# Kernel optimization log

Hardware: AMD Instinct MI355X
Metric: run time of the kernel (lower is better)

## Reference

```python
import jax, jax.numpy as jnp
import numpy as np
from jax import lax

KERNEL_SIZE = 15  # conv padding = kernel_size, kernel width = 2*kernel_size+1


def setup_inputs() -> dict:
    key = jax.random.key(0)
    ks = jax.random.split(key, 11)
    B, T, H, U, KN = 32, 2048, 1024, 1024, 32
    inp = {
        "query": jax.random.normal(ks[0], (1, B, H), dtype=jnp.float32),
        "values": jax.random.normal(ks[1], (B, T, H), dtype=jnp.float32),
        "prev_att": jax.random.uniform(ks[2], (B, 1, T), dtype=jnp.float32),
        "W1_w": jax.random.normal(ks[3], (U, H), dtype=jnp.float32) * 0.02,
        "W1_b": jax.random.normal(ks[4], (U,), dtype=jnp.float32) * 0.02,
        "W2_w": jax.random.normal(ks[5], (U, H), dtype=jnp.float32) * 0.02,
        "W2_b": jax.random.normal(ks[6], (U,), dtype=jnp.float32) * 0.02,
        "V_w": jax.random.normal(ks[7], (1, U), dtype=jnp.float32) * 0.02,
        "V_b": jax.random.normal(ks[8], (1,), dtype=jnp.float32) * 0.02,
        "conv_w": jax.random.normal(ks[9], (KN, 1, 2 * KERNEL_SIZE + 1), dtype=jnp.float32) * 0.02,
        "loc_proj_w": jax.random.normal(ks[10], (U, KN), dtype=jnp.float32) * 0.02,
    }
    return inp


def reference(query, values, prev_att, W1_w, W1_b, W2_w, W2_b, V_w, V_b, conv_w, loc_proj_w):
    # query: [1,B,H] -> [B,H]
    q = jnp.squeeze(query, axis=0)
    hidden_with_time_axis = q[:, None, :]  # [B,1,H]

    # location features: Conv1d over prev attention [B,1,T] -> [B,KN,T]
    loc = lax.conv_general_dilated(
        prev_att, conv_w,
        window_strides=(1,),
        padding=[(KERNEL_SIZE, KERNEL_SIZE)],
        dimension_numbers=("NCH", "OIH", "NCH"),
    )
    # project KN -> units: [B,T,U]
    loc_context = jnp.einsum("bkt,uk->btu", loc, loc_proj_w)

    # W1(values) [B,T,U] + W2(query) [B,1,U] + loc_context [B,T,U]
    sum_1 = (jnp.einsum("bth,uh->btu", values, W1_w) + W1_b
             + jnp.einsum("bh,uh->bu", q, W2_w)[:, None, :] + W2_b
             + loc_context)

    # score: [B,T,1]
    score = jnp.einsum("btu,ou->bto", jnp.tanh(sum_1), V_w) + V_b
    attention_weights = jax.nn.softmax(score, axis=1)  # softmax over time
    context_vector = jnp.sum(attention_weights * values, axis=1)  # [B,H]
    return (context_vector, attention_weights, score)
```

## Files before the change

### kernel.cpp

```cpp
#include <hip/hip_runtime.h>
#include <cstdint>
#include <cstddef>

typedef unsigned short ushort_t;
typedef __attribute__((ext_vector_type(8))) short short8;
typedef __attribute__((ext_vector_type(4))) float floatx4;

#define B_   32
#define T_   2048
#define H_   1024
#define U_   1024
#define KN_  32
#define KEXT 1056
#define BT_  (B_ * T_)

__device__ __forceinline__ unsigned short f2bf(float f) {
    union { float f; unsigned int u; } v; v.f = f;
    unsigned int u = v.u;
    return (unsigned short)((u + 0x7FFFu + ((u >> 16) & 1u)) >> 16);
}
__device__ __forceinline__ float bf2f(unsigned short h) {
    union { unsigned int u; float f; } v; v.u = ((unsigned int)h) << 16;
    return v.f;
}
__device__ __forceinline__ float bflo(unsigned int u) {
    union { unsigned int u; float f; } v; v.u = u << 16; return v.f;
}
__device__ __forceinline__ float bfhi(unsigned int u) {
    union { unsigned int u; float f; } v; v.u = u & 0xffff0000u; return v.f;
}
__device__ __forceinline__ void async_cp16(const void* g, void* l) {
    __builtin_amdgcn_global_load_lds(
        (const __attribute__((address_space(1))) unsigned int*)g,
        (__attribute__((address_space(3))) unsigned int*)l, 16, 0, 0);
}
__device__ __forceinline__ float fast_tanh(float x) {
    float e = __expf(2.0f * x);
    return 1.0f - 2.0f * __builtin_amdgcn_rcpf(e + 1.0f);
}

__global__ void pack_values(const float* __restrict__ values, ushort_t* __restrict__ A) {
    const int tid = threadIdx.x;
    const size_t base = (size_t)blockIdx.x * 8;
#pragma unroll
    for (int r = 0; r < 8; ++r) {
        const size_t row = base + r;
        float4 v = reinterpret_cast<const float4*>(values + row * H_)[tid];
        ushort4 o;
        o.x = f2bf(v.x); o.y = f2bf(v.y); o.z = f2bf(v.z); o.w = f2bf(v.w);
        *reinterpret_cast<ushort4*>(A + row * KEXT + tid * 4) = o;
    }
}

__global__ void conv_pack(const float* __restrict__ prev, const float* __restrict__ convw,
                          ushort_t* __restrict__ A) {
    __shared__ float satt[158];
    __shared__ float sw[KN_ * 31];
    const int tid = threadIdx.x;
    const int b = blockIdx.y, t0 = blockIdx.x * 128;
    for (int i = tid; i < 158; i += 256) {
        int t = t0 - 15 + i;
        satt[i] = (t >= 0 && t < T_) ? prev[b * T_ + t] : 0.0f;
    }
    for (int i = tid; i < KN_ * 31; i += 256) sw[i] = convw[i];
    __syncthreads();
    for (int idx = tid; idx < 128 * KN_; idx += 256) {
        const int k = idx & 31, tl = idx >> 5;
        float acc = 0.0f;
#pragma unroll
        for (int j = 0; j < 31; ++j) acc += satt[tl + j] * sw[k * 31 + j];
        A[(size_t)(b * T_ + t0 + tl) * KEXT + H_ + k] = f2bf(acc);
    }
}

__global__ void pack_w_bias(const float* __restrict__ W1w, const float* __restrict__ locp,
                            const float* __restrict__ W2w, const float* __restrict__ q,
                            const float* __restrict__ W1b, const float* __restrict__ W2b,
                            ushort_t* __restrict__ Bm, float* __restrict__ bias) {
    const int u = blockIdx.x, tid = threadIdx.x;
    float4 v = reinterpret_cast<const float4*>(W1w + (size_t)u * H_)[tid];
    ushort4 o;
    o.x = f2bf(v.x); o.y = f2bf(v.y); o.z = f2bf(v.z); o.w = f2bf(v.w);
    *reinterpret_cast<ushort4*>(Bm + (size_t)u * KEXT + tid * 4) = o;
    if (tid < 8) {
        float4 w = reinterpret_cast<const float4*>(locp + u * KN_)[tid];
        ushort4 o2;
        o2.x = f2bf(w.x); o2.y = f2bf(w.y); o2.z = f2bf(w.z); o2.w = f2bf(w.w);
        *reinterpret_cast<ushort4*>(Bm + (size_t)u * KEXT + H_ + tid * 4) = o2;
    }
    const int lane = tid & 63, wave = tid >> 6;
    const float* wr = W2w + (size_t)u * H_;
    float wv[16];
#pragma unroll
    for (int i = 0; i < 16; ++i) wv[i] = wr[lane + i * 64];
    const float bb = W1b[u] + W2b[u];
#pragma unroll
    for (int j = 0; j < 8; ++j) {
        const int b = wave * 8 + j;
        const float* qr = q + b * H_;
        float acc = 0.0f;
#pragma unroll
        for (int i = 0; i < 16; ++i) acc += wv[i] * qr[lane + i * 64];
#pragma unroll
        for (int off = 32; off >= 1; off >>= 1) acc += __shfl_xor(acc, off, 64);
        if (lane == 0) bias[b * U_ + u] = acc + bb;
    }
}

__global__ __launch_bounds__(256, 2)
void score_gemm(const ushort_t* __restrict__ A, const ushort_t* __restrict__ Bm,
                const float* __restrict__ bias, const float* __restrict__ Vw,
                float* __restrict__ sacc) {
    __shared__ __align__(16) ushort_t lA[128 * 32];
    __shared__ __align__(16) ushort_t lB[128 * 32];
    const int tid  = threadIdx.x;
    const int wave = tid >> 6;
    const int lane = tid & 63;

    const int hid  = blockIdx.x;
    const int xcd  = hid & 7;
    const int slot = hid >> 3;
    const int n_idx = slot & 7;
    const int m_idx = ((slot >> 3) << 3) | xcd;
    const int m0 = m_idx * 128;
    const int n0 = n_idx * 128;

    const int wm = (wave >> 1) * 64;
    const int wn = (wave & 1) * 64;
    const int lr   = lane & 15;
    const int quad = lane >> 4;

    floatx4 acc[4][4] = {};

    const ushort_t* Abase = A + (size_t)m0 * KEXT;
    const ushort_t* Bbase = Bm + (size_t)n0 * KEXT;

    const int chunk0 = wave * 64 + lane;
    const int chunk1 = (4 + wave) * 64 + lane;
    const int r0 = chunk0 >> 2, c0 = chunk0 & 3;
    const int r1 = chunk1 >> 2, c1 = chunk1 & 3;

    for (int kk = 0; kk < 33; ++kk) {
        const int kb = kk * 32;
        async_cp16(Abase + (size_t)r0 * KEXT + kb + c0 * 8, lA + wave * 512);
        async_cp16(Abase + (size_t)r1 * KEXT + kb + c1 * 8, lA + (4 + wave) * 512);
        async_cp16(Bbase + (size_t)r0 * KEXT + kb + c0 * 8, lB + wave * 512);
        async_cp16(Bbase + (size_t)r1 * KEXT + kb + c1 * 8, lB + (4 + wave) * 512);
        __syncthreads();

        short8 af[4], bfr[4];
#pragma unroll
        for (int mi = 0; mi < 4; ++mi)
            af[mi] = *reinterpret_cast<const short8*>(lA + (wm + mi * 16 + lr) * 32 + quad * 8);
#pragma unroll
        for (int ni = 0; ni < 4; ++ni)
            bfr[ni] = *reinterpret_cast<const short8*>(lB + (wn + ni * 16 + lr) * 32 + quad * 8);
#pragma unroll
        for (int mi = 0; mi < 4; ++mi)
#pragma unroll
            for (int ni = 0; ni < 4; ++ni)
                acc[mi][ni] = __builtin_amdgcn_mfma_f32_16x16x32_bf16(af[mi], bfr[ni], acc[mi][ni], 0, 0, 0);
        __syncthreads();
    }

    const int b = m0 >> 11;
    const float* brow = bias + b * U_;
    float vw[4], bv[4];
#pragma unroll
    for (int ni = 0; ni < 4; ++ni) {
        const int u = n0 + wn + ni * 16 + lr;
        vw[ni] = Vw[u];
        bv[ni] = brow[u];
    }
#pragma unroll
    for (int mi = 0; mi < 4; ++mi) {
#pragma unroll
        for (int r = 0; r < 4; ++r) {
            float s = 0.0f;
#pragma unroll
            for (int ni = 0; ni < 4; ++ni)
                s += vw[ni] * fast_tanh(acc[mi][ni][r] + bv[ni]);
            s += __shfl_xor(s, 1, 64);
            s += __shfl_xor(s, 2, 64);
            s += __shfl_xor(s, 4, 64);
            s += __shfl_xor(s, 8, 64);
            if (lr == 0)
                atomicAdd(&sacc[m0 + wm + mi * 16 + quad * 4 + r], s);
        }
    }
}

__global__ void softmax_k(const float* __restrict__ sacc, const float* __restrict__ Vb,
                          float* __restrict__ out) {
    const int b = blockIdx.x, tid = threadIdx.x;
    const int lane = tid & 63, wave = tid >> 6;
    const float vb = Vb[0];
    float v[8], e[8];
    float mx = -1e30f;
#pragma unroll
    for (int j = 0; j < 8; ++j) {
        v[j] = sacc[b * T_ + j * 256 + tid] + vb;
        out[98304 + b * T_ + j * 256 + tid] = v[j];
        mx = fmaxf(mx, v[j]);
    }
#pragma unroll
    for (int off = 32; off >= 1; off >>= 1) mx = fmaxf(mx, __shfl_xor(mx, off, 64));
    __shared__ float sm[4], ss[4];
    if (lane == 0) sm[wave] = mx;
    __syncthreads();
    mx = fmaxf(fmaxf(sm[0], sm[1]), fmaxf(sm[2], sm[3]));
    float sum = 0.0f;
#pragma unroll
    for (int j = 0; j < 8; ++j) { e[j] = __expf(v[j] - mx); sum += e[j]; }
#pragma unroll
    for (int off = 32; off >= 1; off >>= 1) sum += __shfl_xor(sum, off, 64);
    if (lane == 0) ss[wave] = sum;
    __syncthreads();
    sum = ss[0] + ss[1] + ss[2] + ss[3];
    const float inv = 1.0f / sum;
#pragma unroll
    for (int j = 0; j < 8; ++j)
        out[32768 + b * T_ + j * 256 + tid] = e[j] * inv;
}

__global__ void context_k(const ushort_t* __restrict__ A, const float* __restrict__ attn,
                          float* __restrict__ ctx) {
    const int b = blockIdx.y, tc = blockIdx.x, tid = threadIdx.x;
    __shared__ float sa[128];
    if (tid < 128) sa[tid] = attn[b * T_ + tc * 128 + tid];
    __syncthreads();
    const int hh = (tid & 127) * 8;
    const int tp = tid >> 7;
    const ushort_t* base = A + (size_t)(b * T_ + tc * 128 + tp) * KEXT + hh;
    float a[8] = {0, 0, 0, 0, 0, 0, 0, 0};
    for (int t = 0; t < 128; t += 2) {
        const float w = sa[t + tp];
        uint4 u = *reinterpret_cast<const uint4*>(base + (size_t)t * KEXT);
        a[0] += w * bflo(u.x); a[1] += w * bfhi(u.x);
        a[2] += w * bflo(u.y); a[3] += w * bfhi(u.y);
        a[4] += w * bflo(u.z); a[5] += w * bfhi(u.z);
        a[6] += w * bflo(u.w); a[7] += w * bfhi(u.w);
    }
#pragma unroll
    for (int j = 0; j < 8; ++j)
        atomicAdd(&ctx[b * H_ + hh + j], a[j]);
}

extern "C" void kernel_launch(void* const* d_in, const int* in_sizes, int n_in,
                              void* d_out, int out_size, void* d_ws, size_t ws_size,
                              hipStream_t stream) {
    const float* query    = (const float*)d_in[0];
    const float* values   = (const float*)d_in[1];
    const float* prev_att = (const float*)d_in[2];
    const float* W1w      = (const float*)d_in[3];
    const float* W1b      = (const float*)d_in[4];
    const float* W2w      = (const float*)d_in[5];
    const float* W2b      = (const float*)d_in[6];
    const float* Vw       = (const float*)d_in[7];
    const float* Vb       = (const float*)d_in[8];
    const float* convw    = (const float*)d_in[9];
    const float* locp     = (const float*)d_in[10];
    float* out = (float*)d_out;

    char* ws = (char*)d_ws;
    ushort_t* A    = (ushort_t*)(ws);
    ushort_t* Bm   = (ushort_t*)(ws + 138412032);
    float*    bias = (float*)(ws + 140574720);
    float*    sacc = (float*)(ws + 140705792);

    hipMemsetAsync(sacc, 0, BT_ * sizeof(float), stream);
    hipMemsetAsync(out, 0, 32768 * sizeof(float), stream);

    pack_values<<<BT_ / 8, 256, 0, stream>>>(values, A);
    conv_pack<<<dim3(16, 32), 256, 0, stream>>>(prev_att, convw, A);
    pack_w_bias<<<1024, 256, 0, stream>>>(W1w, locp, W2w, query, W1b, W2b, Bm, bias);
    score_gemm<<<4096, 256, 0, stream>>>(A, Bm, bias, Vw, sacc);
    softmax_k<<<32, 256, 0, stream>>>(sacc, Vb, out);
    context_k<<<dim3(16, 32), 256, 0, stream>>>(A, out + 32768, out);
}
```

Baseline: 643.4 us.

## Fuse value packing with conv, swizzle GEMM LDS, and retile context kernel

Merges the values-to-bf16 pack and the location conv into one kernel that writes 16-byte packed stores and computes 8 conv channels per thread. In the score GEMM, the 16-byte chunk index is XOR-swizzled on both the async LDS write and the fragment read to reduce LDS bank conflicts. The context kernel now uses 64-timestep chunks over a 1D grid, doubling block count and atomic adds in exchange for more parallelism. The swizzle has to match exactly between the global_load_lds destination layout and the reads, otherwise MFMA operands come out wrong.

```diff
diff --git a/kernel.cpp b/kernel.cpp
--- a/kernel.cpp
+++ b/kernel.cpp
@@ -14,20 +14,19 @@
 #define KEXT 1056
 #define BT_  (B_ * T_)
 
-__device__ __forceinline__ unsigned short f2bf(float f) {
+__device__ __forceinline__ unsigned int f2bf_u(float f) {
     union { float f; unsigned int u; } v; v.f = f;
     unsigned int u = v.u;
-    return (unsigned short)((u + 0x7FFFu + ((u >> 16) & 1u)) >> 16);
-}
-__device__ __forceinline__ float bf2f(unsigned short h) {
-    union { unsigned int u; float f; } v; v.u = ((unsigned int)h) << 16;
-    return v.f;
+    return (u + 0x7FFFu + ((u >> 16) & 1u)) >> 16;
 }
 __device__ __forceinline__ float bflo(unsigned int u) {
     union { unsigned int u; float f; } v; v.u = u << 16; return v.f;
 }
 __device__ __forceinline__ float bfhi(unsigned int u) {
     union { unsigned int u; float f; } v; v.u = u & 0xffff0000u; return v.f;
+}
+__device__ __forceinline__ unsigned int pack2bf(float a, float b) {
+    return f2bf_u(a) | (f2bf_u(b) << 16);
 }
 __device__ __forceinline__ void async_cp16(const void* g, void* l) {
     __builtin_amdgcn_global_load_lds(
@@ -39,38 +38,53 @@
     return 1.0f - 2.0f * __builtin_amdgcn_rcpf(e + 1.0f);
 }
 
-__global__ void pack_values(const float* __restrict__ values, ushort_t* __restrict__ A) {
+__global__ void pack_all(const float* __restrict__ values, const float* __restrict__ prev,
+                         const float* __restrict__ convw, ushort_t* __restrict__ A) {
+    __shared__ float sw[KN_ * 31];
+    __shared__ float satt[94];
     const int tid = threadIdx.x;
-    const size_t base = (size_t)blockIdx.x * 8;
-#pragma unroll
-    for (int r = 0; r < 8; ++r) {
-        const size_t row = base + r;
-        float4 v = reinterpret_cast<const float4*>(values + row * H_)[tid];
-        ushort4 o;
-        o.x = f2bf(v.x); o.y = f2bf(v.y); o.z = f2bf(v.z); o.w = f2bf(v.w);
-        *reinterpret_cast<ushort4*>(A + row * KEXT + tid * 4) = o;
-    }
-}
-
-__global__ void conv_pack(const float* __restrict__ prev, const float* __restrict__ convw,
-                          ushort_t* __restrict__ A) {
-    __shared__ float satt[158];
-    __shared__ float sw[KN_ * 31];
-    const int tid = threadIdx.x;
-    const int b = blockIdx.y, t0 = blockIdx.x * 128;
-    for (int i = tid; i < 158; i += 256) {
+    const int b  = blockIdx.x >> 5;
+    const int t0 = (blockIdx.x & 31) * 64;
+
+    for (int i = tid; i < KN_ * 31; i += 256) sw[i] = convw[i];
+    for (int i = tid; i < 94; i += 256) {
         int t = t0 - 15 + i;
         satt[i] = (t >= 0 && t < T_) ? prev[b * T_ + t] : 0.0f;
     }
-    for (int i = tid; i < KN_ * 31; i += 256) sw[i] = convw[i];
     __syncthreads();
-    for (int idx = tid; idx < 128 * KN_; idx += 256) {
-        const int k = idx & 31, tl = idx >> 5;
-        float acc = 0.0f;
-#pragma unroll
-        for (int j = 0; j < 31; ++j) acc += satt[tl + j] * sw[k * 31 + j];
-        A[(size_t)(b * T_ + t0 + tl) * KEXT + H_ + k] = f2bf(acc);
-    }
+
+    const int colb = (tid & 127) * 8;
+    const int rp   = tid >> 7;
+#pragma unroll 4
+    for (int pass = 0; pass < 32; ++pass) {
+        const size_t g = (size_t)b * T_ + t0 + pass * 2 + rp;
+        const float* vrow = values + g * H_ + colb;
+        float4 v0 = *reinterpret_cast<const float4*>(vrow);
+        float4 v1 = *reinterpret_cast<const float4*>(vrow + 4);
+        uint4 o;
+        o.x = pack2bf(v0.x, v0.y);
+        o.y = pack2bf(v0.z, v0.w);
+        o.z = pack2bf(v1.x, v1.y);
+        o.w = pack2bf(v1.z, v1.w);
+        *reinterpret_cast<uint4*>(A + g * KEXT + colb) = o;
+    }
+
+    const int tl = tid >> 2;
+    const int k0 = (tid & 3) * 8;
+    float acc[8] = {0, 0, 0, 0, 0, 0, 0, 0};
+#pragma unroll
+    for (int j = 0; j < 31; ++j) {
+        const float p = satt[tl + j];
+#pragma unroll
+        for (int kk = 0; kk < 8; ++kk)
+            acc[kk] += p * sw[(k0 + kk) * 31 + j];
+    }
+    uint4 o;
+    o.x = pack2bf(acc[0], acc[1]);
+    o.y = pack2bf(acc[2], acc[3]);
+    o.z = pack2bf(acc[4], acc[5]);
+    o.w = pack2bf(acc[6], acc[7]);
+    *reinterpret_cast<uint4*>(A + ((size_t)b * T_ + t0 + tl) * KEXT + H_ + k0) = o;
 }
 
 __global__ void pack_w_bias(const float* __restrict__ W1w, const float* __restrict__ locp,
@@ -78,14 +92,19 @@
                             const float* __restrict__ W1b, const float* __restrict__ W2b,
                             ushort_t* __restrict__ Bm, float* __restrict__ bias) {
     const int u = blockIdx.x, tid = threadIdx.x;
-    float4 v = reinterpret_cast<const float4*>(W1w + (size_t)u * H_)[tid];
-    ushort4 o;
-    o.x = f2bf(v.x); o.y = f2bf(v.y); o.z = f2bf(v.z); o.w = f2bf(v.w);
-    *reinterpret_cast<ushort4*>(Bm + (size_t)u * KEXT + tid * 4) = o;
+    {
+        const float* wrow = W1w + (size_t)u * H_ + tid * 4;
+        float4 v = *reinterpret_cast<const float4*>(wrow);
+        ushort4 o;
+        o.x = (ushort_t)f2bf_u(v.x); o.y = (ushort_t)f2bf_u(v.y);
+        o.z = (ushort_t)f2bf_u(v.z); o.w = (ushort_t)f2bf_u(v.w);
+        *reinterpret_cast<ushort4*>(Bm + (size_t)u * KEXT + tid * 4) = o;
+    }
     if (tid < 8) {
         float4 w = reinterpret_cast<const float4*>(locp + u * KN_)[tid];
         ushort4 o2;
-        o2.x = f2bf(w.x); o2.y = f2bf(w.y); o2.z = f2bf(w.z); o2.w = f2bf(w.w);
+        o2.x = (ushort_t)f2bf_u(w.x); o2.y = (ushort_t)f2bf_u(w.y);
+        o2.z = (ushort_t)f2bf_u(w.z); o2.w = (ushort_t)f2bf_u(w.w);
         *reinterpret_cast<ushort4*>(Bm + (size_t)u * KEXT + H_ + tid * 4) = o2;
     }
     const int lane = tid & 63, wave = tid >> 6;
@@ -135,10 +154,12 @@
     const ushort_t* Abase = A + (size_t)m0 * KEXT;
     const ushort_t* Bbase = Bm + (size_t)n0 * KEXT;
 
-    const int chunk0 = wave * 64 + lane;
-    const int chunk1 = (4 + wave) * 64 + lane;
-    const int r0 = chunk0 >> 2, c0 = chunk0 & 3;
-    const int r1 = chunk1 >> 2, c1 = chunk1 & 3;
+    const int s0 = wave * 64 + lane;
+    const int s1 = (4 + wave) * 64 + lane;
+    const int r0 = s0 >> 2, c0 = (s0 & 3) ^ ((s0 >> 3) & 3);
+    const int r1 = s1 >> 2, c1 = (s1 & 3) ^ ((s1 >> 3) & 3);
+
+    const int cxor = (quad ^ ((lr >> 1) & 3)) * 8;
 
     for (int kk = 0; kk < 33; ++kk) {
         const int kb = kk * 32;
@@ -151,10 +172,10 @@
         short8 af[4], bfr[4];
 #pragma unroll
         for (int mi = 0; mi < 4; ++mi)
-            af[mi] = *reinterpret_cast<const short8*>(lA + (wm + mi * 16 + lr) * 32 + quad * 8);
+            af[mi] = *reinterpret_cast<const short8*>(lA + (wm + mi * 16 + lr) * 32 + cxor);
 #pragma unroll
         for (int ni = 0; ni < 4; ++ni)
-            bfr[ni] = *reinterpret_cast<const short8*>(lB + (wn + ni * 16 + lr) * 32 + quad * 8);
+            bfr[ni] = *reinterpret_cast<const short8*>(lB + (wn + ni * 16 + lr) * 32 + cxor);
 #pragma unroll
         for (int mi = 0; mi < 4; ++mi)
 #pragma unroll
@@ -225,15 +246,16 @@
 
 __global__ void context_k(const ushort_t* __restrict__ A, const float* __restrict__ attn,
                           float* __restrict__ ctx) {
-    const int b = blockIdx.y, tc = blockIdx.x, tid = threadIdx.x;
-    __shared__ float sa[128];
-    if (tid < 128) sa[tid] = attn[b * T_ + tc * 128 + tid];
+    const int b = blockIdx.x >> 5, tc = blockIdx.x & 31, tid = threadIdx.x;
+    __shared__ float sa[64];
+    if (tid < 64) sa[tid] = attn[b * T_ + tc * 64 + tid];
     __syncthreads();
     const int hh = (tid & 127) * 8;
     const int tp = tid >> 7;
-    const ushort_t* base = A + (size_t)(b * T_ + tc * 128 + tp) * KEXT + hh;
+    const ushort_t* base = A + (size_t)(b * T_ + tc * 64 + tp) * KEXT + hh;
     float a[8] = {0, 0, 0, 0, 0, 0, 0, 0};
-    for (int t = 0; t < 128; t += 2) {
+#pragma unroll 4
+    for (int t = 0; t < 64; t += 2) {
         const float w = sa[t + tp];
         uint4 u = *reinterpret_cast<const uint4*>(base + (size_t)t * KEXT);
         a[0] += w * bflo(u.x); a[1] += w * bfhi(u.x);
@@ -271,10 +293,9 @@
     hipMemsetAsync(sacc, 0, BT_ * sizeof(float), stream);
     hipMemsetAsync(out, 0, 32768 * sizeof(float), stream);
 
-    pack_values<<<BT_ / 8, 256, 0, stream>>>(values, A);
-    conv_pack<<<dim3(16, 32), 256, 0, stream>>>(prev_att, convw, A);
+    pack_all<<<1024, 256, 0, stream>>>(values, prev_att, convw, A);
     pack_w_bias<<<1024, 256, 0, stream>>>(W1w, locp, W2w, query, W1b, W2b, Bm, bias);
     score_gemm<<<4096, 256, 0, stream>>>(A, Bm, bias, Vw, sacc);
     softmax_k<<<32, 256, 0, stream>>>(sacc, Vb, out);
-    context_k<<<dim3(16, 32), 256, 0, stream>>>(A, out + 32768, out);
-}
+    context_k<<<1024, 256, 0, stream>>>(A, out + 32768, out);
+}
```

Result: slower. 670.9 us (+4.3%).
